# Performance work log

Measured on AMD Instinct MI355X. Metric: run time of the kernel, lower is better.

The kernel has to match this reference:

```python
import jax, jax.numpy as jnp
import numpy as np

D_MODEL = 4096
HIDDEN = 16384
N_TOKENS = 4096


def dequant4(packed, scales):
    """Unpack 4-bit signed values (2 per byte, high nibble first) and apply per-row scales.
    packed: [d_out, d_in//2] ints in [0,256); scales: [d_out, 1].
    Returns [d_out, d_in] float weights."""
    hi = (packed >> 4) - 8          # even columns
    lo = (packed & 15) - 8          # odd columns
    d_out = packed.shape[0]
    w = jnp.stack([hi, lo], axis=-1).reshape(d_out, -1).astype(scales.dtype)
    return w * scales


def setup_inputs() -> dict:
    key = jax.random.key(0)
    k1, k2, k3, k4, k5 = jax.random.split(key, 5)
    x = jax.random.normal(k1, (N_TOKENS, D_MODEL), dtype=jnp.float32)
    fc1_packed = jax.random.randint(k2, (HIDDEN, D_MODEL // 2), 0, 256, dtype=jnp.int32)
    fc1_scales = jax.random.uniform(k3, (HIDDEN, 1), dtype=jnp.float32) * 0.02 + 1e-4
    fc2_packed = jax.random.randint(k4, (D_MODEL, HIDDEN // 2), 0, 256, dtype=jnp.int32)
    fc2_scales = jax.random.uniform(k5, (D_MODEL, 1), dtype=jnp.float32) * 0.02 + 1e-4
    return {"x": x, "fc1_packed": fc1_packed, "fc1_scales": fc1_scales,
            "fc2_packed": fc2_packed, "fc2_scales": fc2_scales}


def reference(x, fc1_packed, fc1_scales, fc2_packed, fc2_scales):
    W1 = dequant4(fc1_packed, fc1_scales)   # [HIDDEN, D_MODEL]
    W2 = dequant4(fc2_packed, fc2_scales)   # [D_MODEL, HIDDEN]
    h = jax.nn.gelu(x @ W1.T)                # [N, HIDDEN]
    return h @ W2.T                          # [N, D_MODEL]
```

## Files before the change

### kernel.cpp

```cpp
#include <hip/hip_runtime.h>
#include <cstdint>

typedef unsigned short u16;
typedef unsigned int   u32;

#define D_MODEL 4096
#define HIDDEN  16384
#define NTOK    4096

typedef short bf16x8  __attribute__((ext_vector_type(8)));
typedef float floatx4 __attribute__((ext_vector_type(4)));

typedef __attribute__((address_space(1))) u32 gu32;
typedef __attribute__((address_space(3))) u32 lu32;

__device__ __forceinline__ void gl_lds16(const void* g, void* l) {
  __builtin_amdgcn_global_load_lds((gu32*)g, (lu32*)l, 16, 0, 0);
}

__device__ __forceinline__ u16 f32_bf16_rne(float f) {
  union { float f; u32 u; } c; c.f = f;
  u32 u = c.u;
  return (u16)((u + 0x7FFFu + ((u >> 16) & 1u)) >> 16);
}

__device__ __forceinline__ float gelu_tanh(float x) {
  float inner = 0.7978845608028654f * fmaf(0.044715f * x * x, x, x);
  float e  = __expf(2.0f * inner);
  float th = 1.0f - 2.0f / (e + 1.0f);
  return 0.5f * x * (1.0f + th);
}

__global__ void __launch_bounds__(256) cvt_f32_bf16(const float4* __restrict__ in,
                                                    ushort4* __restrict__ out) {
  int i = blockIdx.x * 256 + threadIdx.x;
  float4 v = in[i];
  ushort4 o;
  o.x = f32_bf16_rne(v.x);
  o.y = f32_bf16_rne(v.y);
  o.z = f32_bf16_rne(v.z);
  o.w = f32_bf16_rne(v.w);
  out[i] = o;
}

template <int K>
__global__ void __launch_bounds__(256)
dequant_w(const int4* __restrict__ Bp, const float* __restrict__ Bsc,
          uint4* __restrict__ W, int rowOffset) {
  const int i = blockIdx.x * 256 + threadIdx.x;
  const int row_local = i / (K / 8);
  const float s = Bsc[rowOffset + row_local];
  const float m8s = -8.0f * s;
  int4 p = Bp[(size_t)rowOffset * (K / 8) + i];
  int b[4] = {p.x, p.y, p.z, p.w};
  union { u16 e[8]; uint4 q; } u;
#pragma unroll
  for (int j = 0; j < 4; ++j) {
    u.e[2 * j]     = f32_bf16_rne(fmaf((float)(b[j] >> 4), s, m8s));
    u.e[2 * j + 1] = f32_bf16_rne(fmaf((float)(b[j] & 15), s, m8s));
  }
  W[i] = u.q;
}


#define STAGE(T, SEG)                                                          \
  do {                                                                         \
    const size_t kof_ = (size_t)(T) * 64 + (size_t)(((SEG) >> 1) * 32);        \
    char* d_ = ldsw + (((T) & 1) << 16) + ((SEG) << 14) + (w2 << 10);          \
    if ((SEG) & 1) {                                                           \
      gl_lds16(bst0 + kof_, d_);                                               \
      gl_lds16(bst1 + kof_, d_ + 1024);                                        \
    } else {                                                                   \
      gl_lds16(ast0 + kof_, d_);                                               \
      gl_lds16(ast1 + kof_, d_ + 1024);                                        \
    }                                                                          \
  } while (0)

#define PHASE(BB, MH, S, RDB, VME, STG)                                        \
  do {                                                                         \
    const char* ab_ = ldsr + ((BB) << 16) + ((S) * 32768);                     \
    _Pragma("unroll")                                                          \
    for (int f_ = 0; f_ < 4; ++f_)                                             \
      af[f_] = *(const bf16x8*)(ab_ + ((MH) * 4 + f_) * 1024 + aoff);          \
    if (RDB) {                                                                 \
      _Pragma("unroll")                                                        \
      for (int f_ = 0; f_ < 4; ++f_)                                           \
        bf[f_] = *(const bf16x8*)(ab_ + 16384 + f_ * 1024 + boff);             \
    }                                                                          \
    STG;                                                                       \
    __builtin_amdgcn_s_barrier();                                              \
    asm volatile("s_waitcnt lgkmcnt(0)" ::: "memory");                         \
    __builtin_amdgcn_sched_barrier(0);                                         \
    __builtin_amdgcn_s_setprio(1);                                             \
    _Pragma("unroll")                                                          \
    for (int f_ = 0; f_ < 4; ++f_) {                                           \
      _Pragma("unroll")                                                        \
      for (int n_ = 0; n_ < 4; ++n_)                                           \
        acc[(MH) * 4 + f_][n_] = __builtin_amdgcn_mfma_f32_16x16x32_bf16(      \
            af[f_], bf[n_], acc[(MH) * 4 + f_][n_], 0, 0, 0);                  \
    }                                                                          \
    __builtin_amdgcn_s_setprio(0);                                             \
    if ((VME) == 6) asm volatile("s_waitcnt vmcnt(6)" ::: "memory");           \
    if ((VME) == 0) asm volatile("s_waitcnt vmcnt(0)" ::: "memory");           \
    __builtin_amdgcn_s_barrier();                                              \
  } while (0)

template <int K, int NLD, bool GELU>
__global__ void __launch_bounds__(512, 2)
gemm_nt8(const u16* __restrict__ A, const u16* __restrict__ B,
         u16* __restrict__ Cb, float* __restrict__ Cf, int nbase) {
  __shared__ __align__(16) u16 lds[2 * 4 * 8192];
  char* ldsw = (char*)lds;
  const char* ldsr = (const char*)lds;

  const int tid  = threadIdx.x;
  const int lane = tid & 63;
  const int wave = tid >> 6;
  const int quad = lane >> 4;
  const int l16  = lane & 15;
  const int wm   = wave >> 2;
  const int wn   = wave & 3;

  const int gx  = gridDim.x;
  const int nwg = gx * gridDim.y;
  const int orig = blockIdx.y * gx + blockIdx.x;
  const int q = nwg >> 3, r = nwg & 7;
  const int xcd = orig & 7, lid = orig >> 3;
  const int wgid = (xcd < r ? xcd * (q + 1) : r * (q + 1) + (xcd - r) * q) + lid;
  const int n0 = (wgid % gx) * 256;
  const int m0 = (wgid / gx) * 256;

  const int w2   = wave * 2;
  const int rl   = lane >> 2;
  const int kcol = ((lane & 3) * 8) ^ ((lane & 32) ? 16 : 0);
  const u16* ast0 = A + (size_t)(m0 + w2 * 16 + rl) * K + kcol;
  const u16* ast1 = ast0 + (size_t)16 * K;
  const u16* bst0 = B + (size_t)(n0 + w2 * 16 + rl) * K + kcol;
  const u16* bst1 = bst0 + (size_t)16 * K;

  u32 pa = (u32)((wm * 128 + l16) * 64 + quad * 16);
  const u32 aoff = pa ^ (((pa >> 9) & 1) << 5);
  u32 pb = (u32)((wn * 64 + l16) * 64 + quad * 16);
  const u32 boff = pb ^ (((pb >> 9) & 1) << 5);

  floatx4 acc[8][4];
#pragma unroll
  for (int i = 0; i < 8; ++i)
#pragma unroll
    for (int j = 0; j < 4; ++j) acc[i][j] = (floatx4){0.f, 0.f, 0.f, 0.f};

  bf16x8 af[4], bf[4];

  STAGE(0, 0); STAGE(0, 1); STAGE(0, 2); STAGE(0, 3);
  STAGE(1, 0); STAGE(1, 1); STAGE(1, 3);
  asm volatile("s_waitcnt vmcnt(6)" ::: "memory");
  __builtin_amdgcn_s_barrier();

  const int KT = K / 64;
  for (int t = 0; t < KT - 2; t += 2) {
    PHASE(0, 0, 0, 1, -1, STAGE(t + 1, 2));
    PHASE(0, 1, 0, 0, -1, STAGE(t + 2, 1));
    PHASE(0, 1, 1, 1, -1, STAGE(t + 2, 0));
    PHASE(0, 0, 1, 0,  6, STAGE(t + 2, 3));
    PHASE(1, 0, 0, 1, -1, STAGE(t + 2, 2));
    PHASE(1, 1, 0, 0, -1, STAGE(t + 3, 1));
    PHASE(1, 1, 1, 1, -1, STAGE(t + 3, 0));
    PHASE(1, 0, 1, 0,  6, STAGE(t + 3, 3));
  }
  PHASE(0, 0, 0, 1, -1, STAGE(KT - 1, 2));
  PHASE(0, 1, 0, 0, -1, (void)0);
  PHASE(0, 1, 1, 1, -1, (void)0);
  PHASE(0, 0, 1, 0,  0, (void)0);
  PHASE(1, 0, 0, 1, -1, (void)0);
  PHASE(1, 1, 0, 0, -1, (void)0);
  PHASE(1, 1, 1, 1, -1, (void)0);
  PHASE(1, 0, 1, 0, -1, (void)0);

  const int crow0 = m0 + wm * 128 + quad * 4;
  const int ccol0 = nbase + n0 + wn * 64 + l16;
#pragma unroll
  for (int mf = 0; mf < 8; ++mf) {
#pragma unroll
    for (int rr = 0; rr < 4; ++rr) {
      const size_t row = (size_t)(crow0 + mf * 16 + rr);
#pragma unroll
      for (int nf = 0; nf < 4; ++nf) {
        float v = acc[mf][nf][rr];
        const size_t idx = row * NLD + (size_t)(ccol0 + nf * 16);
        if constexpr (GELU) {
          Cb[idx] = f32_bf16_rne(gelu_tanh(v));
        } else {
          Cf[idx] = v;
        }
      }
    }
  }
}

#undef PHASE
#undef STAGE

template <int K, int N, bool GELU>
__global__ void __launch_bounds__(256)
gemm_dq(const u16* __restrict__ A, const int* __restrict__ Bp,
        const float* __restrict__ Bsc, u16* __restrict__ Cb, float* __restrict__ Cf) {
  __shared__ __align__(16) u16 As[128 * 32];
  __shared__ __align__(16) u16 Bs[128 * 32];

  const int tid  = threadIdx.x;
  const int lane = tid & 63;
  const int wave = tid >> 6;
  const int quad = lane >> 4;
  const int l16  = lane & 15;
  const int wm = wave >> 1, wn = wave & 1;

  const int n0 = blockIdx.x * 128;
  const int m0 = blockIdx.y * 128;

  const int brow  = tid >> 1;
  const int bhalf = tid & 1;
  const float s   = Bsc[n0 + brow];
  const float m8s = -8.0f * s;
  const int4* bp  = (const int4*)(Bp + (size_t)(n0 + brow) * (K / 2)) + bhalf * 2;
  u16* blds = Bs + (brow >> 4) * 512 + (2 * bhalf) * 128 + (brow & 15) * 8;

  const u16* ag = A + (size_t)(m0 + l16) * K + (size_t)quad * 8;
  u16* alds0 = As + (wave * 2 + 0) * 512;
  u16* alds1 = As + (wave * 2 + 1) * 512;

  floatx4 acc[4][4];
#pragma unroll
  for (int i = 0; i < 4; ++i)
#pragma unroll
    for (int j = 0; j < 4; ++j)
      acc[i][j] = (floatx4){0.f, 0.f, 0.f, 0.f};

  const int KT = K / 32;
  for (int kt = 0; kt < KT; ++kt) {
    int4 w0 = bp[(size_t)kt * 4 + 0];
    int4 w1 = bp[(size_t)kt * 4 + 1];
    __syncthreads();
    gl_lds16(ag + (size_t)(wave * 2 + 0) * 16 * K + kt * 32, alds0);
    gl_lds16(ag + (size_t)(wave * 2 + 1) * 16 * K + kt * 32, alds1);
    int wv[8] = {w0.x, w0.y, w0.z, w0.w, w1.x, w1.y, w1.z, w1.w};
    union { u16 e[16]; uint4 q[2]; } u;
#pragma unroll
    for (int j = 0; j < 8; ++j) {
      int v = wv[j];
      u.e[2 * j]     = f32_bf16_rne(fmaf((float)(v >> 4), s, m8s));
      u.e[2 * j + 1] = f32_bf16_rne(fmaf((float)(v & 15), s, m8s));
    }
    *(uint4*)(blds)       = u.q[0];
    *(uint4*)(blds + 128) = u.q[1];
    __syncthreads();

    bf16x8 af[4], bf[4];
#pragma unroll
    for (int im = 0; im < 4; ++im)
      af[im] = *(const bf16x8*)(As + (wm * 4 + im) * 512 + quad * 128 + l16 * 8);
#pragma unroll
    for (int in = 0; in < 4; ++in)
      bf[in] = *(const bf16x8*)(Bs + (wn * 4 + in) * 512 + quad * 128 + l16 * 8);
#pragma unroll
    for (int im = 0; im < 4; ++im)
#pragma unroll
      for (int in = 0; in < 4; ++in)
        acc[im][in] = __builtin_amdgcn_mfma_f32_16x16x32_bf16(af[im], bf[in], acc[im][in], 0, 0, 0);
  }

#pragma unroll
  for (int im = 0; im < 4; ++im) {
#pragma unroll
    for (int r = 0; r < 4; ++r) {
      const int row = m0 + wm * 64 + im * 16 + quad * 4 + r;
#pragma unroll
      for (int in = 0; in < 4; ++in) {
        const int col = n0 + wn * 64 + in * 16 + l16;
        float v = acc[im][in][r];
        if constexpr (GELU) {
          Cb[(size_t)row * N + col] = f32_bf16_rne(gelu_tanh(v));
        } else {
          Cf[(size_t)row * N + col] = v;
        }
      }
    }
  }
}

extern "C" void kernel_launch(void* const* d_in, const int* in_sizes, int n_in,
                              void* d_out, int out_size, void* d_ws, size_t ws_size,
                              hipStream_t stream) {
  const float* x   = (const float*)d_in[0];
  const int*   f1p = (const int*)d_in[1];
  const float* f1s = (const float*)d_in[2];
  const int*   f2p = (const int*)d_in[3];
  const float* f2s = (const float*)d_in[4];
  float* out = (float*)d_out;

  const size_t xb_bytes = (size_t)NTOK * D_MODEL * 2;
  const size_t h_bytes  = (size_t)NTOK * HIDDEN * 2;
  const size_t base     = xb_bytes + h_bytes;
  if (ws_size < base) return;

  u16* xb = (u16*)d_ws;
  u16* h  = xb + (size_t)NTOK * D_MODEL;

  cvt_f32_bf16<<<(NTOK * D_MODEL) / 1024, 256, 0, stream>>>((const float4*)x, (ushort4*)xb);

  const size_t avail = ws_size - base;
  int NC1 = 0;
  for (int c = HIDDEN; c >= 1024; c >>= 1)
    if ((size_t)c * D_MODEL * 2 <= avail) { NC1 = c; break; }

  if (NC1 == 0) {
    gemm_dq<D_MODEL, HIDDEN, true>
        <<<dim3(HIDDEN / 128, NTOK / 128), 256, 0, stream>>>(xb, f1p, f1s, h, nullptr);
    gemm_dq<HIDDEN, D_MODEL, false>
        <<<dim3(D_MODEL / 128, NTOK / 128), 256, 0, stream>>>(h, f2p, f2s, nullptr, out);
    return;
  }

  u16* Wbuf = h + (size_t)NTOK * HIDDEN;
  const int NC2 = NC1 / 4;

  for (int r = 0; r < HIDDEN; r += NC1) {
    dequant_w<D_MODEL><<<(NC1 * (D_MODEL / 8)) / 256, 256, 0, stream>>>(
        (const int4*)f1p, f1s, (uint4*)Wbuf, r);
    gemm_nt8<D_MODEL, HIDDEN, true>
        <<<dim3(NC1 / 256, NTOK / 256), 512, 0, stream>>>(xb, Wbuf, h, nullptr, r);
  }

  for (int r = 0; r < D_MODEL; r += NC2) {
    dequant_w<HIDDEN><<<(NC2 * (HIDDEN / 8)) / 256, 256, 0, stream>>>(
        (const int4*)f2p, f2s, (uint4*)Wbuf, r);
    gemm_nt8<HIDDEN, D_MODEL, false>
        <<<dim3(NC2 / 256, NTOK / 256), 512, 0, stream>>>(h, Wbuf, nullptr, out, r);
  }
}
```

Before: 1.504 ms.

## Fuse 4-bit weight dequantization into GEMM mainloop via packed nibble staging

Replaces the separate bf16 weight dequantization kernels and chunked GEMM launches with a byte-packing repack kernel, followed by GEMMs that load packed nibbles into registers and dequantize them into LDS inside the pipelined mainloop. This removes the full bf16 weight materialization round trip through global memory and the per-chunk launch loop. The cost is extra VALU work and register pressure inside the MFMA loop, plus a reworked vmcnt wait schedule that must stay correct.

```diff
diff --git a/kernel.cpp b/kernel.cpp
--- a/kernel.cpp
+++ b/kernel.cpp
@@ -22,6 +22,12 @@
   union { float f; u32 u; } c; c.f = f;
   u32 u = c.u;
   return (u16)((u + 0x7FFFu + ((u >> 16) & 1u)) >> 16);
+}
+
+__device__ __forceinline__ u32 cvt_pk_bf16(float lo, float hi) {
+  u32 r;
+  asm("v_cvt_pk_bf16_f32 %0, %1, %2" : "=v"(r) : "v"(lo), "v"(hi));
+  return r;
 }
 
 __device__ __forceinline__ float gelu_tanh(float x) {
@@ -43,40 +49,57 @@
   out[i] = o;
 }
 
-template <int K>
 __global__ void __launch_bounds__(256)
-dequant_w(const int4* __restrict__ Bp, const float* __restrict__ Bsc,
-          uint4* __restrict__ W, int rowOffset) {
-  const int i = blockIdx.x * 256 + threadIdx.x;
-  const int row_local = i / (K / 8);
-  const float s = Bsc[rowOffset + row_local];
-  const float m8s = -8.0f * s;
-  int4 p = Bp[(size_t)rowOffset * (K / 8) + i];
-  int b[4] = {p.x, p.y, p.z, p.w};
-  union { u16 e[8]; uint4 q; } u;
-#pragma unroll
-  for (int j = 0; j < 4; ++j) {
-    u.e[2 * j]     = f32_bf16_rne(fmaf((float)(b[j] >> 4), s, m8s));
-    u.e[2 * j + 1] = f32_bf16_rne(fmaf((float)(b[j] & 15), s, m8s));
-  }
-  W[i] = u.q;
-}
-
-
-#define STAGE(T, SEG)                                                          \
+repack_nib(const int4* __restrict__ in, uint4* __restrict__ out) {
+  const size_t i = (size_t)blockIdx.x * 256 + threadIdx.x;
+  int4 a = in[4 * i + 0], b = in[4 * i + 1], c = in[4 * i + 2], d = in[4 * i + 3];
+  uint4 o;
+  o.x = (u32)(a.x & 255) | ((u32)(a.y & 255) << 8) | ((u32)(a.z & 255) << 16) | ((u32)(a.w & 255) << 24);
+  o.y = (u32)(b.x & 255) | ((u32)(b.y & 255) << 8) | ((u32)(b.z & 255) << 16) | ((u32)(b.w & 255) << 24);
+  o.z = (u32)(c.x & 255) | ((u32)(c.y & 255) << 8) | ((u32)(c.z & 255) << 16) | ((u32)(c.w & 255) << 24);
+  o.w = (u32)(d.x & 255) | ((u32)(d.y & 255) << 8) | ((u32)(d.z & 255) << 16) | ((u32)(d.w & 255) << 24);
+  out[i] = o;
+}
+
+__device__ __forceinline__ void wr8(char* d, u32 v, float s, float m8s) {
+  u32 b0 = v & 0xFFu, b1 = (v >> 8) & 0xFFu, b2 = (v >> 16) & 0xFFu, b3 = v >> 24;
+  uint4 q;
+  q.x = cvt_pk_bf16(fmaf((float)(b0 >> 4), s, m8s), fmaf((float)(b0 & 15u), s, m8s));
+  q.y = cvt_pk_bf16(fmaf((float)(b1 >> 4), s, m8s), fmaf((float)(b1 & 15u), s, m8s));
+  q.z = cvt_pk_bf16(fmaf((float)(b2 >> 4), s, m8s), fmaf((float)(b2 & 15u), s, m8s));
+  q.w = cvt_pk_bf16(fmaf((float)(b3 >> 4), s, m8s), fmaf((float)(b3 & 15u), s, m8s));
+  *(uint4*)d = q;
+}
+
+
+#define VMW(N) asm volatile("s_waitcnt vmcnt(" #N ")" ::: "memory")
+#define FEN()  asm volatile("" ::: "memory")
+
+#define ASTG(T, SEG)                                                           \
   do {                                                                         \
     const size_t kof_ = (size_t)(T) * 64 + (size_t)(((SEG) >> 1) * 32);        \
     char* d_ = ldsw + (((T) & 1) << 16) + ((SEG) << 14) + (w2 << 10);          \
-    if ((SEG) & 1) {                                                           \
-      gl_lds16(bst0 + kof_, d_);                                               \
-      gl_lds16(bst1 + kof_, d_ + 1024);                                        \
-    } else {                                                                   \
-      gl_lds16(ast0 + kof_, d_);                                               \
-      gl_lds16(ast1 + kof_, d_ + 1024);                                        \
-    }                                                                          \
+    gl_lds16(ast0 + kof_, d_);                                                 \
+    gl_lds16(ast1 + kof_, d_ + 1024);                                          \
   } while (0)
 
-#define PHASE(BB, MH, S, RDB, VME, STG)                                        \
+#define BLOAD(T, DST)                                                          \
+  do {                                                                         \
+    DST.x = bn0[(T) * 8];                                                      \
+    DST.y = bn0[(T) * 8 + 4];                                                  \
+    DST.z = bn1[(T) * 8];                                                      \
+    DST.w = bn1[(T) * 8 + 4];                                                  \
+  } while (0)
+
+#define BDEQ(T, KS, V0, V1)                                                    \
+  do {                                                                         \
+    char* d_ = ldsw + (((T) & 1) << 16) + ((1 + 2 * (KS)) << 14) +             \
+               (w2 << 10) + lane * 16;                                         \
+    wr8(d_, (V0), s0, m8s0);                                                   \
+    wr8(d_ + 1024, (V1), s1, m8s1);                                            \
+  } while (0)
+
+#define PH(BB, MH, S, RDB, STG)                                                \
   do {                                                                         \
     const char* ab_ = ldsr + ((BB) << 16) + ((S) * 32768);                     \
     _Pragma("unroll")                                                          \
@@ -100,15 +123,14 @@
             af[f_], bf[n_], acc[(MH) * 4 + f_][n_], 0, 0, 0);                  \
     }                                                                          \
     __builtin_amdgcn_s_setprio(0);                                             \
-    if ((VME) == 6) asm volatile("s_waitcnt vmcnt(6)" ::: "memory");           \
-    if ((VME) == 0) asm volatile("s_waitcnt vmcnt(0)" ::: "memory");           \
     __builtin_amdgcn_s_barrier();                                              \
   } while (0)
 
-template <int K, int NLD, bool GELU>
+template <int K, int N, bool GELU>
 __global__ void __launch_bounds__(512, 2)
-gemm_nt8(const u16* __restrict__ A, const u16* __restrict__ B,
-         u16* __restrict__ Cb, float* __restrict__ Cf, int nbase) {
+gemm_nt8(const u16* __restrict__ A, const u32* __restrict__ Bnib,
+         const float* __restrict__ Bsc, u16* __restrict__ Cb,
+         float* __restrict__ Cf) {
   __shared__ __align__(16) u16 lds[2 * 4 * 8192];
   char* ldsw = (char*)lds;
   const char* ldsr = (const char*)lds;
@@ -135,8 +157,14 @@
   const int kcol = ((lane & 3) * 8) ^ ((lane & 32) ? 16 : 0);
   const u16* ast0 = A + (size_t)(m0 + w2 * 16 + rl) * K + kcol;
   const u16* ast1 = ast0 + (size_t)16 * K;
-  const u16* bst0 = B + (size_t)(n0 + w2 * 16 + rl) * K + kcol;
-  const u16* bst1 = bst0 + (size_t)16 * K;
+
+  const int brow0 = n0 + w2 * 16 + rl;
+  const u32* bn0 = Bnib + (size_t)brow0 * (K / 8) + (kcol >> 3);
+  const u32* bn1 = Bnib + (size_t)(brow0 + 16) * (K / 8) + (kcol >> 3);
+  const float s0 = Bsc[brow0];
+  const float s1 = Bsc[brow0 + 16];
+  const float m8s0 = -8.0f * s0;
+  const float m8s1 = -8.0f * s1;
 
   u32 pa = (u32)((wm * 128 + l16) * 64 + quad * 16);
   const u32 aoff = pa ^ (((pa >> 9) & 1) << 5);
@@ -150,34 +178,57 @@
     for (int j = 0; j < 4; ++j) acc[i][j] = (floatx4){0.f, 0.f, 0.f, 0.f};
 
   bf16x8 af[4], bf[4];
-
-  STAGE(0, 0); STAGE(0, 1); STAGE(0, 2); STAGE(0, 3);
-  STAGE(1, 0); STAGE(1, 1); STAGE(1, 3);
-  asm volatile("s_waitcnt vmcnt(6)" ::: "memory");
+  uint4 bt0, bt1, bq0, bq1, bq0n, bq1n;
+
+  ASTG(0, 0); ASTG(0, 2); ASTG(1, 0);
+  BLOAD(0, bt0); BLOAD(1, bt1); BLOAD(2, bq0); BLOAD(3, bq1);
+  FEN();
+  VMW(8);
+  BDEQ(0, 0, bt0.x, bt0.z);
+  BDEQ(0, 1, bt0.y, bt0.w);
+  BDEQ(1, 0, bt1.x, bt1.z);
+  BDEQ(1, 1, bt1.y, bt1.w);
+  asm volatile("s_waitcnt lgkmcnt(0)" ::: "memory");
   __builtin_amdgcn_s_barrier();
 
   const int KT = K / 64;
-  for (int t = 0; t < KT - 2; t += 2) {
-    PHASE(0, 0, 0, 1, -1, STAGE(t + 1, 2));
-    PHASE(0, 1, 0, 0, -1, STAGE(t + 2, 1));
-    PHASE(0, 1, 1, 1, -1, STAGE(t + 2, 0));
-    PHASE(0, 0, 1, 0,  6, STAGE(t + 2, 3));
-    PHASE(1, 0, 0, 1, -1, STAGE(t + 2, 2));
-    PHASE(1, 1, 0, 0, -1, STAGE(t + 3, 1));
-    PHASE(1, 1, 1, 1, -1, STAGE(t + 3, 0));
-    PHASE(1, 0, 1, 0,  6, STAGE(t + 3, 3));
-  }
-  PHASE(0, 0, 0, 1, -1, STAGE(KT - 1, 2));
-  PHASE(0, 1, 0, 0, -1, (void)0);
-  PHASE(0, 1, 1, 1, -1, (void)0);
-  PHASE(0, 0, 1, 0,  0, (void)0);
-  PHASE(1, 0, 0, 1, -1, (void)0);
-  PHASE(1, 1, 0, 0, -1, (void)0);
-  PHASE(1, 1, 1, 1, -1, (void)0);
-  PHASE(1, 0, 1, 0, -1, (void)0);
+  for (int t = 0; t < KT - 4; t += 2) {
+    PH(0, 0, 0, 1, ASTG(t + 1, 2); BLOAD(t + 4, bq0n); FEN());
+    PH(0, 1, 0, 0, VMW(8); BDEQ(t + 2, 0, bq0.x, bq0.z));
+    PH(0, 1, 1, 1, ASTG(t + 2, 0); FEN());
+    PH(0, 0, 1, 0, VMW(8); BDEQ(t + 2, 1, bq0.y, bq0.w));
+    PH(1, 0, 0, 1, ASTG(t + 2, 2); BLOAD(t + 5, bq1n); FEN());
+    PH(1, 1, 0, 0, VMW(8); BDEQ(t + 3, 0, bq1.x, bq1.z));
+    PH(1, 1, 1, 1, ASTG(t + 3, 0); FEN());
+    PH(1, 0, 1, 0, VMW(8); BDEQ(t + 3, 1, bq1.y, bq1.w));
+    bq0 = bq0n;
+    bq1 = bq1n;
+  }
+  {
+    const int t = KT - 4;
+    PH(0, 0, 0, 1, ASTG(t + 1, 2); FEN());
+    PH(0, 1, 0, 0, VMW(8); BDEQ(t + 2, 0, bq0.x, bq0.z));
+    PH(0, 1, 1, 1, ASTG(t + 2, 0); FEN());
+    PH(0, 0, 1, 0, VMW(4); BDEQ(t + 2, 1, bq0.y, bq0.w));
+    PH(1, 0, 0, 1, ASTG(t + 2, 2); FEN());
+    PH(1, 1, 0, 0, VMW(4); BDEQ(t + 3, 0, bq1.x, bq1.z));
+    PH(1, 1, 1, 1, ASTG(t + 3, 0); FEN());
+    PH(1, 0, 1, 0, VMW(4); BDEQ(t + 3, 1, bq1.y, bq1.w));
+  }
+  {
+    const int t = KT - 2;
+    PH(0, 0, 0, 1, ASTG(t + 1, 2); FEN());
+    PH(0, 1, 0, 0, VMW(4));
+    PH(0, 1, 1, 1, (void)0);
+    PH(0, 0, 1, 0, VMW(2));
+    PH(1, 0, 0, 1, VMW(0));
+    PH(1, 1, 0, 0, (void)0);
+    PH(1, 1, 1, 1, (void)0);
+    PH(1, 0, 1, 0, (void)0);
+  }
 
   const int crow0 = m0 + wm * 128 + quad * 4;
-  const int ccol0 = nbase + n0 + wn * 64 + l16;
+  const int ccol0 = n0 + wn * 64 + l16;
 #pragma unroll
   for (int mf = 0; mf < 8; ++mf) {
 #pragma unroll
@@ -186,7 +237,7 @@
 #pragma unroll
       for (int nf = 0; nf < 4; ++nf) {
         float v = acc[mf][nf][rr];
-        const size_t idx = row * NLD + (size_t)(ccol0 + nf * 16);
+        const size_t idx = row * N + (size_t)(ccol0 + nf * 16);
         if constexpr (GELU) {
           Cb[idx] = f32_bf16_rne(gelu_tanh(v));
         } else {
@@ -197,8 +248,12 @@
   }
 }
 
-#undef PHASE
-#undef STAGE
+#undef PH
+#undef BDEQ
+#undef BLOAD
+#undef ASTG
+#undef VMW
+#undef FEN
 
 template <int K, int N, bool GELU>
 __global__ void __launch_bounds__(256)
@@ -297,9 +352,10 @@
   const float* f2s = (const float*)d_in[4];
   float* out = (float*)d_out;
 
-  const size_t xb_bytes = (size_t)NTOK * D_MODEL * 2;
-  const size_t h_bytes  = (size_t)NTOK * HIDDEN * 2;
-  const size_t base     = xb_bytes + h_bytes;
+  const size_t xb_bytes  = (size_t)NTOK * D_MODEL * 2;
+  const size_t h_bytes   = (size_t)NTOK * HIDDEN * 2;
+  const size_t nib_bytes = (size_t)HIDDEN * D_MODEL / 2;
+  const size_t base      = xb_bytes + h_bytes;
   if (ws_size < base) return;
 
   u16* xb = (u16*)d_ws;
@@ -307,12 +363,7 @@
 
   cvt_f32_bf16<<<(NTOK * D_MODEL) / 1024, 256, 0, stream>>>((const float4*)x, (ushort4*)xb);
 
-  const size_t avail = ws_size - base;
-  int NC1 = 0;
-  for (int c = HIDDEN; c >= 1024; c >>= 1)
-    if ((size_t)c * D_MODEL * 2 <= avail) { NC1 = c; break; }
-
-  if (NC1 == 0) {
+  if (ws_size < base + 2 * nib_bytes) {
     gemm_dq<D_MODEL, HIDDEN, true>
         <<<dim3(HIDDEN / 128, NTOK / 128), 256, 0, stream>>>(xb, f1p, f1s, h, nullptr);
     gemm_dq<HIDDEN, D_MODEL, false>
@@ -320,20 +371,15 @@
     return;
   }
 
-  u16* Wbuf = h + (size_t)NTOK * HIDDEN;
-  const int NC2 = NC1 / 4;
-
-  for (int r = 0; r < HIDDEN; r += NC1) {
-    dequant_w<D_MODEL><<<(NC1 * (D_MODEL / 8)) / 256, 256, 0, stream>>>(
-        (const int4*)f1p, f1s, (uint4*)Wbuf, r);
-    gemm_nt8<D_MODEL, HIDDEN, true>
-        <<<dim3(NC1 / 256, NTOK / 256), 512, 0, stream>>>(xb, Wbuf, h, nullptr, r);
-  }
-
-  for (int r = 0; r < D_MODEL; r += NC2) {
-    dequant_w<HIDDEN><<<(NC2 * (HIDDEN / 8)) / 256, 256, 0, stream>>>(
-        (const int4*)f2p, f2s, (uint4*)Wbuf, r);
-    gemm_nt8<HIDDEN, D_MODEL, false>
-        <<<dim3(NC2 / 256, NTOK / 256), 512, 0, stream>>>(h, Wbuf, nullptr, out, r);
-  }
-}
+  u32* nib1 = (u32*)(h + (size_t)NTOK * HIDDEN);
+  u32* nib2 = nib1 + nib_bytes / 4;
+
+  const int nblk = (int)((size_t)HIDDEN * (D_MODEL / 2) / 16 / 256);
+  repack_nib<<<nblk, 256, 0, stream>>>((const int4*)f1p, (uint4*)nib1);
+  repack_nib<<<nblk, 256, 0, stream>>>((const int4*)f2p, (uint4*)nib2);
+
+  gemm_nt8<D_MODEL, HIDDEN, true>
+      <<<dim3(HIDDEN / 256, NTOK / 256), 512, 0, stream>>>(xb, nib1, f1s, h, nullptr);
+  gemm_nt8<HIDDEN, D_MODEL, false>
+      <<<dim3(D_MODEL / 256, NTOK / 256), 512, 0, stream>>>(h, nib2, f2s, nullptr, out);
+}
```

Result: faster. 1.386 ms (-7.8%).
